# Kernel tuning notes

Measured on AMD Instinct MI355X. Metric: run time of the kernel, lower is better.

## Reference

```python
import jax, jax.numpy as jnp
import numpy as np

N = 1_000_000      # nodes
E = 8_000_000      # edges per relation
IN, HID, OUT = 25, 10, 5
GAT_SLOPE = 0.2    # GATv2Conv negative_slope default
ACT_SLOPE = 0.1    # module's LeakyReLU(0.1)


def setup_inputs() -> dict:
    key = jax.random.key(0)
    ks = jax.random.split(key, 40)
    d = {}
    d["x"] = jax.random.normal(ks[0], (N, IN), dtype=jnp.float32)
    for i, s in enumerate("psv"):
        d[f"edge_index_{s}"] = jax.random.randint(ks[1 + i], (2, E), 0, N, dtype=jnp.int32)
    # GATv2Conv params per relation: lin_l (source), lin_r (target), attention vec, bias
    k = 4
    for s in "psv":
        d[f"Wl_{s}"] = jax.random.normal(ks[k], (IN, OUT), jnp.float32) * 0.2; k += 1
        d[f"Wr_{s}"] = jax.random.normal(ks[k], (IN, OUT), jnp.float32) * 0.2; k += 1
        d[f"att_{s}"] = jax.random.normal(ks[k], (OUT,), jnp.float32) * 0.2; k += 1
        d[f"b_{s}"] = jnp.zeros((OUT,), jnp.float32)
    # projection: Linear(15,10) -> LeakyReLU(0.1) -> Linear(10,5)
    d["Wp1"] = jax.random.normal(ks[k], (3 * OUT, 2 * OUT), jnp.float32) * 0.2; k += 1
    d["bp1"] = jnp.zeros((2 * OUT,), jnp.float32)
    d["Wp2"] = jax.random.normal(ks[k], (2 * OUT, OUT), jnp.float32) * 0.2; k += 1
    d["bp2"] = jnp.zeros((OUT,), jnp.float32)
    # classifier: Linear(5,5) -> LeakyReLU(0.1) -> Linear(5,2)
    d["Wc1"] = jax.random.normal(ks[k], (OUT, OUT), jnp.float32) * 0.2; k += 1
    d["bc1"] = jnp.zeros((OUT,), jnp.float32)
    d["Wc2"] = jax.random.normal(ks[k], (OUT, 2), jnp.float32) * 0.2; k += 1
    d["bc2"] = jnp.zeros((2,), jnp.float32)
    return d


def lrelu(v, slope):
    return jnp.where(v >= 0, v, slope * v)


def gatv2_conv(x, edge_index, Wl, Wr, att, bias):
    """Single-head GATv2Conv with self-loops (PyG defaults)."""
    loops = jnp.arange(N, dtype=edge_index.dtype)
    src = jnp.concatenate([edge_index[0], loops])  # message sources j
    dst = jnp.concatenate([edge_index[1], loops])  # message targets i
    xl = x @ Wl  # [N, OUT] source transform (also message value)
    xr = x @ Wr  # [N, OUT] target transform
    # per-edge attention logits: a^T LeakyReLU(xl[j] + xr[i])
    e = lrelu(xl[src] + xr[dst], GAT_SLOPE) @ att  # [E+N]
    # segment softmax over incoming edges of each target node
    m = jax.ops.segment_max(e, dst, num_segments=N)
    ex = jnp.exp(e - m[dst])
    denom = jax.ops.segment_sum(ex, dst, num_segments=N)
    alpha = ex / denom[dst]
    out = jax.ops.segment_sum(alpha[:, None] * xl[src], dst, num_segments=N)
    return out + bias


def reference(x, edge_index_p, edge_index_s, edge_index_v,
              Wl_p, Wr_p, att_p, b_p,
              Wl_s, Wr_s, att_s, b_s,
              Wl_v, Wr_v, att_v, b_v,
              Wp1, bp1, Wp2, bp2, Wc1, bc1, Wc2, bc2):
    xp = lrelu(gatv2_conv(x, edge_index_p, Wl_p, Wr_p, att_p, b_p), ACT_SLOPE)
    xs = lrelu(gatv2_conv(x, edge_index_s, Wl_s, Wr_s, att_s, b_s), ACT_SLOPE)
    xv = lrelu(gatv2_conv(x, edge_index_v, Wl_v, Wr_v, att_v, b_v), ACT_SLOPE)
    h = jnp.concatenate([xp, xs, xv], axis=1)            # [N, 15]
    h = lrelu(h @ Wp1 + bp1, ACT_SLOPE) @ Wp2 + bp2      # projection (dropout=0)
    h = lrelu(h @ Wc1 + bc1, ACT_SLOPE) @ Wc2 + bc2      # classifier
    return h  # [N, 2]
```

## Files before the change

### kernel.cpp

```cpp
#include <hip/hip_runtime.h>

static constexpr int KIN  = 25;
static constexpr int KOUT = 5;
static constexpr int NBLK = 512;
static constexpr int BTH  = 1024;
static constexpr int BSH  = 9;
static constexpr int NPB  = 1 << BSH;
static constexpr int NBH  = 2048;
static constexpr int BROW = NBH + 1;
static constexpr int CAP  = 5120;

__global__ __launch_bounds__(256) void k_node1(
    const float* __restrict__ x,
    const float* __restrict__ Wl, const float* __restrict__ Wr,
    float* __restrict__ xl8, float* __restrict__ xr5, int n)
{
    __shared__ float sWl[KIN * KOUT];
    __shared__ float sWr[KIN * KOUT];
    __shared__ float sx[256 * KIN];

    const int tid = threadIdx.x;
    if (tid < KIN * KOUT) { sWl[tid] = Wl[tid]; sWr[tid] = Wr[tid]; }

    const int base = blockIdx.x * 256;
    const int cnt  = min(256, n - base);
    const size_t xbase = (size_t)base * KIN;
    for (int i = tid; i < cnt * KIN; i += 256) sx[i] = x[xbase + i];
    __syncthreads();

    if (tid >= cnt) return;
    const int node = base + tid;

    float xls[KOUT] = {0.f, 0.f, 0.f, 0.f, 0.f};
    float xrs[KOUT] = {0.f, 0.f, 0.f, 0.f, 0.f};
    const float* xp = &sx[tid * KIN];
#pragma unroll
    for (int i = 0; i < KIN; ++i) {
        const float xv = xp[i];
#pragma unroll
        for (int o = 0; o < KOUT; ++o) {
            xls[o] += xv * sWl[i * KOUT + o];
            xrs[o] += xv * sWr[i * KOUT + o];
        }
    }

    const size_t n8 = (size_t)node * 8;
    float4 v4;
    v4.x = xls[0]; v4.y = xls[1]; v4.z = xls[2]; v4.w = xls[3];
    *(float4*)(xl8 + n8) = v4;
    xl8[n8 + 4] = xls[4];
    const size_t n5 = (size_t)node * 5;
#pragma unroll
    for (int o = 0; o < KOUT; ++o) xr5[n5 + o] = xrs[o];
}

__global__ __launch_bounds__(256) void k_node3(
    const float* __restrict__ x,
    const float* __restrict__ Wl0, const float* __restrict__ Wr0,
    const float* __restrict__ Wl1, const float* __restrict__ Wr1,
    const float* __restrict__ Wl2, const float* __restrict__ Wr2,
    float* __restrict__ xl8, float* __restrict__ xr5,
    int n)
{
    __shared__ float sWl[3][KIN * KOUT];
    __shared__ float sWr[3][KIN * KOUT];
    __shared__ float sx[256 * KIN];

    const int tid = threadIdx.x;
    if (tid < KIN * KOUT) {
        sWl[0][tid] = Wl0[tid]; sWr[0][tid] = Wr0[tid];
        sWl[1][tid] = Wl1[tid]; sWr[1][tid] = Wr1[tid];
        sWl[2][tid] = Wl2[tid]; sWr[2][tid] = Wr2[tid];
    }

    const int base = blockIdx.x * 256;
    const int cnt  = min(256, n - base);
    const size_t xbase = (size_t)base * KIN;
    for (int i = tid; i < cnt * KIN; i += 256) sx[i] = x[xbase + i];
    __syncthreads();

    if (tid >= cnt) return;
    const int node = base + tid;

    float xls[3][KOUT] = {};
    float xrs[3][KOUT] = {};
    const float* xp = &sx[tid * KIN];
#pragma unroll
    for (int i = 0; i < KIN; ++i) {
        const float xv = xp[i];
#pragma unroll
        for (int r = 0; r < 3; ++r)
#pragma unroll
            for (int o = 0; o < KOUT; ++o) {
                xls[r][o] += xv * sWl[r][i * KOUT + o];
                xrs[r][o] += xv * sWr[r][i * KOUT + o];
            }
    }

#pragma unroll
    for (int r = 0; r < 3; ++r) {
        const size_t n8 = (size_t)r * n * 8 + (size_t)node * 8;
        float4 v4;
        v4.x = xls[r][0]; v4.y = xls[r][1]; v4.z = xls[r][2]; v4.w = xls[r][3];
        *(float4*)(xl8 + n8) = v4;
        xl8[n8 + 4] = xls[r][4];
        const size_t n5 = (size_t)r * n * 5 + (size_t)node * 5;
#pragma unroll
        for (int o = 0; o < KOUT; ++o) xr5[n5 + o] = xrs[r][o];
    }
}

__global__ __launch_bounds__(BTH) void k_hist3(
    const int* __restrict__ d0p, const int* __restrict__ d1p,
    const int* __restrict__ d2p, int E, int NB, int* __restrict__ hist3)
{
    __shared__ int h[NBH];
    const int rel = blockIdx.y, b = blockIdx.x, tid = threadIdx.x;
    const int* dst = (rel == 0) ? d0p : (rel == 1 ? d1p : d2p);
    int* hist_blk = hist3 + (size_t)rel * NBLK * NBH;

    for (int i = tid; i < NB; i += BTH) h[i] = 0;
    __syncthreads();
    const int chunk = (E + NBLK - 1) / NBLK;
    const int eb = b * chunk, ee = min(E, eb + chunk);
    for (int i = eb + tid; i < ee; i += BTH)
        atomicAdd(&h[dst[i] >> BSH], 1);
    __syncthreads();
    for (int i = tid; i < NB; i += BTH) hist_blk[b * NBH + i] = h[i];
}

__global__ __launch_bounds__(256) void k_sumoffs3(
    int* __restrict__ hist3, int NB, int* __restrict__ totals3)
{
    const int rel = blockIdx.y;
    int* hist_blk = hist3 + (size_t)rel * NBLK * NBH;
    int* totals   = totals3 + rel * NBH;
    const int i = blockIdx.x * 256 + threadIdx.x;
    if (i >= NB) return;
    int s = 0;
    for (int b = 0; b < NBLK; ++b) {
        const int t = hist_blk[b * NBH + i];
        hist_blk[b * NBH + i] = s;
        s += t;
    }
    totals[i] = s;
}

__global__ __launch_bounds__(1024) void k_scan3(
    const int* __restrict__ totals3, int E, int NB, int* __restrict__ base3)
{
    __shared__ int s[1024];
    const int rel = blockIdx.x;
    const int* totals = totals3 + rel * NBH;
    int* base = base3 + rel * BROW;

    const int t = threadIdx.x;
    const int i0 = 2 * t, i1 = 2 * t + 1;
    const int t0 = (i0 < NB) ? totals[i0] : 0;
    const int t1 = (i1 < NB) ? totals[i1] : 0;
    const int pair = t0 + t1;
    s[t] = pair;
    __syncthreads();
    for (int off = 1; off < 1024; off <<= 1) {
        int v = (t >= off) ? s[t - off] : 0;
        __syncthreads();
        s[t] += v;
        __syncthreads();
    }
    const int excl = s[t] - pair;
    base[i0] = excl;
    base[i1] = excl + t0;
    if (t == 1023) base[NBH] = E;
}

__global__ __launch_bounds__(BTH) void k_scatter3(
    const int* __restrict__ s0p, const int* __restrict__ s1p,
    const int* __restrict__ s2p,
    const int* __restrict__ d0p, const int* __restrict__ d1p,
    const int* __restrict__ d2p,
    int E, int NB,
    const int* __restrict__ hist3, const int* __restrict__ base3,
    int* __restrict__ rs3)
{
    __shared__ int cur[NBH];
    const int rel = blockIdx.y, b = blockIdx.x, tid = threadIdx.x;
    const int* src = (rel == 0) ? s0p : (rel == 1 ? s1p : s2p);
    const int* dst = (rel == 0) ? d0p : (rel == 1 ? d1p : d2p);
    const int* hist_blk = hist3 + (size_t)rel * NBLK * NBH;
    const int* base = base3 + rel * BROW;
    int* rs = rs3 + (size_t)rel * E;

    for (int i = tid; i < NB; i += BTH)
        cur[i] = base[i] + hist_blk[b * NBH + i];
    __syncthreads();
    const int chunk = (E + NBLK - 1) / NBLK;
    const int eb = b * chunk, ee = min(E, eb + chunk);
    for (int i = eb + tid; i < ee; i += BTH) {
        const int d = dst[i];
        const int bkt = d >> BSH;
        const int pos = atomicAdd(&cur[bkt], 1);
        rs[pos] = (src[i] << BSH) | (d & (NPB - 1));
    }
}

template <int NREL>
__global__ __launch_bounds__(256) void k_gather4(
    const int* __restrict__ rs3, const int* __restrict__ base3,
    const float* __restrict__ xl8a, const float* __restrict__ xr5a,
    const float* __restrict__ at0, const float* __restrict__ at1,
    const float* __restrict__ at2,
    const float* __restrict__ bi0, const float* __restrict__ bi1,
    const float* __restrict__ bi2,
    float* __restrict__ xouta, int n, int E)
{
    __shared__ float acc[NPB][6];
    __shared__ float xrw[NPB * 5];
    __shared__ int   cur[NPB];
    __shared__ int   sorted[CAP];
    __shared__ int   sc[256];

    const int bx  = blockIdx.x;
    const int rel = (NREL == 1) ? 0 : bx % NREL;
    const int bkt = (NREL == 1) ? bx : bx / NREL;

    const int*   rs   = rs3 + (size_t)rel * E;
    const int*   base = base3 + rel * BROW;
    const float* xl8  = xl8a + (size_t)rel * 8 * n;
    const float* xr5  = xr5a + (size_t)rel * 5 * n;
    const float* att  = (rel == 0) ? at0 : (rel == 1 ? at1 : at2);
    const float* bias = (rel == 0) ? bi0 : (rel == 1 ? bi1 : bi2);
    float*       xout = xouta + (size_t)rel * 5 * n;

    const int tid = threadIdx.x;
    const int node0 = bkt << BSH;
    const int nn = min(NPB, n - node0);

    for (int i = tid; i < NPB * 6; i += 256) ((float*)acc)[i] = 0.f;
    for (int i = tid; i < nn * 5; i += 256) xrw[i] = xr5[(size_t)node0 * 5 + i];
    for (int i = tid; i < NPB; i += 256) cur[i] = 0;
    __syncthreads();

    const float a0 = att[0], a1 = att[1], a2 = att[2], a3 = att[3], a4 = att[4];
    const int eb = base[bkt], ee = base[bkt + 1];
    const int seg = ee - eb;

    if (seg > 0 && seg <= CAP) {
        for (int i = eb + tid; i < ee; i += 256)
            atomicAdd(&cur[rs[i] & (NPB - 1)], 1);
        __syncthreads();
        const int h0 = cur[2 * tid], h1 = cur[2 * tid + 1];
        const int pair = h0 + h1;
        sc[tid] = pair;
        __syncthreads();
        for (int off = 1; off < 256; off <<= 1) {
            const int v = (tid >= off) ? sc[tid - off] : 0;
            __syncthreads();
            sc[tid] += v;
            __syncthreads();
        }
        const int excl = sc[tid] - pair;
        cur[2 * tid] = excl;
        cur[2 * tid + 1] = excl + h0;
        __syncthreads();
        for (int i = eb + tid; i < ee; i += 256) {
            const int v = rs[i];
            const int p = atomicAdd(&cur[v & (NPB - 1)], 1);
            sorted[p] = v;
        }
        __syncthreads();
        const int C  = (seg + 255) / 256;
        const int s0 = tid * C;
        const int s1 = min(seg, s0 + C);
        int curdl = -1;
        float A0 = 0.f, A1 = 0.f, A2 = 0.f, A3 = 0.f, A4 = 0.f, A5 = 0.f;
        float xr0 = 0.f, xr1 = 0.f, xr2 = 0.f, xr3 = 0.f, xr4 = 0.f;
        for (int i = s0; i < s1; ++i) {
            const int v  = sorted[i];
            const int dl = v & (NPB - 1);
            const int s  = v >> BSH;
            const size_t s8 = (size_t)s * 8;
            const float4 xs = *(const float4*)(xl8 + s8);
            const float  xs4 = xl8[s8 + 4];
            if (dl != curdl) {
                if (curdl >= 0) {
                    atomicAdd(&acc[curdl][0], A0);
                    atomicAdd(&acc[curdl][1], A1);
                    atomicAdd(&acc[curdl][2], A2);
                    atomicAdd(&acc[curdl][3], A3);
                    atomicAdd(&acc[curdl][4], A4);
                    atomicAdd(&acc[curdl][5], A5);
                }
                curdl = dl;
                A0 = A1 = A2 = A3 = A4 = A5 = 0.f;
                const float* xr = &xrw[dl * 5];
                xr0 = xr[0]; xr1 = xr[1]; xr2 = xr[2]; xr3 = xr[3]; xr4 = xr[4];
            }
            float t, lg = 0.f;
            t = xs.x + xr0; t = (t >= 0.f) ? t : 0.2f * t; lg += t * a0;
            t = xs.y + xr1; t = (t >= 0.f) ? t : 0.2f * t; lg += t * a1;
            t = xs.z + xr2; t = (t >= 0.f) ? t : 0.2f * t; lg += t * a2;
            t = xs.w + xr3; t = (t >= 0.f) ? t : 0.2f * t; lg += t * a3;
            t = xs4  + xr4; t = (t >= 0.f) ? t : 0.2f * t; lg += t * a4;
            const float w = __expf(lg);
            A0 += w * xs.x; A1 += w * xs.y; A2 += w * xs.z;
            A3 += w * xs.w; A4 += w * xs4;  A5 += w;
        }
        if (curdl >= 0) {
            atomicAdd(&acc[curdl][0], A0);
            atomicAdd(&acc[curdl][1], A1);
            atomicAdd(&acc[curdl][2], A2);
            atomicAdd(&acc[curdl][3], A3);
            atomicAdd(&acc[curdl][4], A4);
            atomicAdd(&acc[curdl][5], A5);
        }
        __syncthreads();
    } else if (seg > CAP) {
        for (int i = eb + tid; i < ee; i += 256) {
            const int v  = rs[i];
            const int s  = v >> BSH;
            const int dl = v & (NPB - 1);
            const size_t s8 = (size_t)s * 8;
            const float4 xs = *(const float4*)(xl8 + s8);
            const float  xs4 = xl8[s8 + 4];
            const float* xr = &xrw[dl * 5];
            float t, lg = 0.f;
            t = xs.x + xr[0]; t = (t >= 0.f) ? t : 0.2f * t; lg += t * a0;
            t = xs.y + xr[1]; t = (t >= 0.f) ? t : 0.2f * t; lg += t * a1;
            t = xs.z + xr[2]; t = (t >= 0.f) ? t : 0.2f * t; lg += t * a2;
            t = xs.w + xr[3]; t = (t >= 0.f) ? t : 0.2f * t; lg += t * a3;
            t = xs4  + xr[4]; t = (t >= 0.f) ? t : 0.2f * t; lg += t * a4;
            const float w = __expf(lg);
            atomicAdd(&acc[dl][0], w * xs.x);
            atomicAdd(&acc[dl][1], w * xs.y);
            atomicAdd(&acc[dl][2], w * xs.z);
            atomicAdd(&acc[dl][3], w * xs.w);
            atomicAdd(&acc[dl][4], w * xs4);
            atomicAdd(&acc[dl][5], w);
        }
        __syncthreads();
    } else {
        __syncthreads();
    }

    const float b0 = bias[0], b1 = bias[1], b2 = bias[2], b3 = bias[3], b4 = bias[4];
    for (int l = tid; l < nn; l += 256) {
        const int node = node0 + l;
        const size_t s8 = (size_t)node * 8;
        const float4 xs = *(const float4*)(xl8 + s8);
        const float  xs4 = xl8[s8 + 4];
        const float* xr = &xrw[l * 5];

        float t, lg = 0.f;
        t = xs.x + xr[0]; t = (t >= 0.f) ? t : 0.2f * t; lg += t * a0;
        t = xs.y + xr[1]; t = (t >= 0.f) ? t : 0.2f * t; lg += t * a1;
        t = xs.z + xr[2]; t = (t >= 0.f) ? t : 0.2f * t; lg += t * a2;
        t = xs.w + xr[3]; t = (t >= 0.f) ? t : 0.2f * t; lg += t * a3;
        t = xs4  + xr[4]; t = (t >= 0.f) ? t : 0.2f * t; lg += t * a4;
        const float w = __expf(lg);

        const size_t d5 = (size_t)node * 5;
        const float inv = 1.0f / (acc[l][5] + w);
        float v;
        v = (acc[l][0] + w * xs.x) * inv + b0; xout[d5 + 0] = (v >= 0.f) ? v : 0.1f * v;
        v = (acc[l][1] + w * xs.y) * inv + b1; xout[d5 + 1] = (v >= 0.f) ? v : 0.1f * v;
        v = (acc[l][2] + w * xs.z) * inv + b2; xout[d5 + 2] = (v >= 0.f) ? v : 0.1f * v;
        v = (acc[l][3] + w * xs.w) * inv + b3; xout[d5 + 3] = (v >= 0.f) ? v : 0.1f * v;
        v = (acc[l][4] + w * xs4 ) * inv + b4; xout[d5 + 4] = (v >= 0.f) ? v : 0.1f * v;
    }
}

__global__ __launch_bounds__(256) void k_mlp(
    const float* __restrict__ xp, const float* __restrict__ xs,
    const float* __restrict__ xv,
    const float* __restrict__ Wp1, const float* __restrict__ bp1,
    const float* __restrict__ Wp2, const float* __restrict__ bp2,
    const float* __restrict__ Wc1, const float* __restrict__ bc1,
    const float* __restrict__ Wc2, const float* __restrict__ bc2,
    float* __restrict__ out, int n)
{
    __shared__ float sW[257];
    const int tid = threadIdx.x;
    if (tid < 150) sW[tid] = Wp1[tid];
    if (tid < 10)  sW[150 + tid] = bp1[tid];
    if (tid < 50)  sW[160 + tid] = Wp2[tid];
    if (tid < 5)   sW[210 + tid] = bp2[tid];
    if (tid < 25)  sW[215 + tid] = Wc1[tid];
    if (tid < 5)   sW[240 + tid] = bc1[tid];
    if (tid < 10)  sW[245 + tid] = Wc2[tid];
    if (tid < 2)   sW[255 + tid] = bc2[tid];
    __syncthreads();

    const int node = blockIdx.x * 256 + tid;
    if (node >= n) return;
    const size_t n5 = (size_t)node * KOUT;

    float h[15];
#pragma unroll
    for (int k = 0; k < 5; ++k) {
        h[k]      = xp[n5 + k];
        h[5 + k]  = xs[n5 + k];
        h[10 + k] = xv[n5 + k];
    }

    float t1[10];
#pragma unroll
    for (int o = 0; o < 10; ++o) {
        float a = sW[150 + o];
#pragma unroll
        for (int i = 0; i < 15; ++i) a += h[i] * sW[i * 10 + o];
        t1[o] = (a >= 0.f) ? a : 0.1f * a;
    }

    float t2[5];
#pragma unroll
    for (int o = 0; o < 5; ++o) {
        float a = sW[210 + o];
#pragma unroll
        for (int i = 0; i < 10; ++i) a += t1[i] * sW[160 + i * 5 + o];
        t2[o] = a;
    }

    float t3[5];
#pragma unroll
    for (int o = 0; o < 5; ++o) {
        float a = sW[240 + o];
#pragma unroll
        for (int i = 0; i < 5; ++i) a += t2[i] * sW[215 + i * 5 + o];
        t3[o] = (a >= 0.f) ? a : 0.1f * a;
    }

    float o0 = sW[255], o1 = sW[256];
#pragma unroll
    for (int i = 0; i < 5; ++i) {
        o0 += t3[i] * sW[245 + i * 2 + 0];
        o1 += t3[i] * sW[245 + i * 2 + 1];
    }
    out[(size_t)node * 2 + 0] = o0;
    out[(size_t)node * 2 + 1] = o1;
}

extern "C" void kernel_launch(void* const* d_in, const int* in_sizes, int n_in,
                              void* d_out, int out_size, void* d_ws, size_t ws_size,
                              hipStream_t stream)
{
    const float* x = (const float*)d_in[0];
    const int n = in_sizes[0] / KIN;
    const int E = in_sizes[1] / 2;
    const int NB = (n + NPB - 1) >> BSH;

    const int* ei[3] = { (const int*)d_in[1], (const int*)d_in[2], (const int*)d_in[3] };
    const float *Wl[3], *Wr[3], *att[3], *bias[3];
    for (int r = 0; r < 3; ++r) {
        const int base = 4 + r * 4;
        Wl[r]   = (const float*)d_in[base + 0];
        Wr[r]   = (const float*)d_in[base + 1];
        att[r]  = (const float*)d_in[base + 2];
        bias[r] = (const float*)d_in[base + 3];
    }
    const float* Wp1 = (const float*)d_in[16];
    const float* bp1 = (const float*)d_in[17];
    const float* Wp2 = (const float*)d_in[18];
    const float* bp2 = (const float*)d_in[19];
    const float* Wc1 = (const float*)d_in[20];
    const float* bc1 = (const float*)d_in[21];
    const float* Wc2 = (const float*)d_in[22];
    const float* bc2 = (const float*)d_in[23];

    const size_t intsA = (size_t)3 * E + 3 * NBH + 3 * BROW;
    const size_t need_A = ((size_t)54 * n + intsA) * 4;
    const bool fused = ws_size >= need_A;

    float* ws   = (float*)d_ws;
    float* xout = ws;
    float* xl8  = ws + (size_t)15 * n;
    float* xr5  = xl8 + (fused ? (size_t)24 * n : (size_t)8 * n);
    int*   rs3  = (int*)(xr5 + (fused ? (size_t)15 * n : (size_t)5 * n));
    int*   totals3 = rs3 + (fused ? (size_t)3 * E : (size_t)E);
    int*   base3   = totals3 + (fused ? 3 * NBH : NBH);
    int*   hist3   = (int*)(xout + (size_t)10 * n);

    const int nb_node = (n + 255) / 256;
    const int nb_cols = (NB + 255) / 256;

    if (fused) {
        k_node3<<<nb_node, 256, 0, stream>>>(x, Wl[0], Wr[0], Wl[1], Wr[1],
                                             Wl[2], Wr[2], xl8, xr5, n);
        k_hist3   <<<dim3(NBLK, 3),    BTH,  0, stream>>>(ei[0] + E, ei[1] + E,
                                                          ei[2] + E, E, NB, hist3);
        k_sumoffs3<<<dim3(nb_cols, 3), 256,  0, stream>>>(hist3, NB, totals3);
        k_scan3   <<<3,                1024, 0, stream>>>(totals3, E, NB, base3);
        k_scatter3<<<dim3(NBLK, 3),    BTH,  0, stream>>>(
            ei[0], ei[1], ei[2], ei[0] + E, ei[1] + E, ei[2] + E,
            E, NB, hist3, base3, rs3);
        k_gather4<3><<<3 * NB, 256, 0, stream>>>(
            rs3, base3, xl8, xr5,
            att[0], att[1], att[2], bias[0], bias[1], bias[2],
            xout, n, E);
    } else {
        for (int r = 0; r < 3; ++r) {
            float* xo = xout + (size_t)r * 5 * n;
            k_node1<<<nb_node, 256, 0, stream>>>(x, Wl[r], Wr[r], xl8, xr5, n);
            k_hist3   <<<dim3(NBLK, 1),    BTH,  0, stream>>>(ei[r] + E, ei[r] + E,
                                                              ei[r] + E, E, NB, hist3);
            k_sumoffs3<<<dim3(nb_cols, 1), 256,  0, stream>>>(hist3, NB, totals3);
            k_scan3   <<<1,                1024, 0, stream>>>(totals3, E, NB, base3);
            k_scatter3<<<dim3(NBLK, 1),    BTH,  0, stream>>>(
                ei[r], ei[r], ei[r], ei[r] + E, ei[r] + E, ei[r] + E,
                E, NB, hist3, base3, rs3);
            k_gather4<1><<<NB, 256, 0, stream>>>(
                rs3, base3, xl8, xr5,
                att[r], att[r], att[r], bias[r], bias[r], bias[r],
                xo, n, E);
        }
    }

    k_mlp<<<nb_node, 256, 0, stream>>>(xout, xout + (size_t)5 * n, xout + (size_t)10 * n,
                                       Wp1, bp1, Wp2, bp2, Wc1, bc1, Wc2, bc2,
                                       (float*)d_out, n);
}
```

Measured before the change: 1.116 ms.

## Fuse node transform into histogram kernel and vectorize edge loads

Merges the node-projection kernel into the histogram kernel as extra blocks, so the compute-bound projection can overlap with the atomic-bound histogram and one launch is removed. Histogram and scatter now read dst/src as int4, with chunks rounded to multiples of four so the vector loads stay aligned. The gather block mapping changes from interleaved relations to relation-major order. Risks include the fused kernel's larger shared footprint and 1024-thread blocks for the node work lowering occupancy, and 4x-unrolled scatter atomics changing contention patterns.

```diff
diff --git a/kernel.cpp b/kernel.cpp
--- a/kernel.cpp
+++ b/kernel.cpp
@@ -54,79 +54,91 @@
     for (int o = 0; o < KOUT; ++o) xr5[n5 + o] = xrs[o];
 }
 
-__global__ __launch_bounds__(256) void k_node3(
+__global__ __launch_bounds__(BTH) void k_histnode(
+    const int* __restrict__ d0p, const int* __restrict__ d1p,
+    const int* __restrict__ d2p, int E, int NB, int* __restrict__ hist3,
     const float* __restrict__ x,
     const float* __restrict__ Wl0, const float* __restrict__ Wr0,
     const float* __restrict__ Wl1, const float* __restrict__ Wr1,
     const float* __restrict__ Wl2, const float* __restrict__ Wr2,
-    float* __restrict__ xl8, float* __restrict__ xr5,
-    int n)
-{
-    __shared__ float sWl[3][KIN * KOUT];
-    __shared__ float sWr[3][KIN * KOUT];
-    __shared__ float sx[256 * KIN];
-
-    const int tid = threadIdx.x;
+    float* __restrict__ xl8, float* __restrict__ xr5, int n, int NNB)
+{
+    __shared__ float smem[7424];
+    const int y = blockIdx.y, bx = blockIdx.x, tid = threadIdx.x;
+
+    if (bx < NBLK) {
+        int* h = (int*)smem;
+        const int* dst = (y == 0) ? d0p : (y == 1 ? d1p : d2p);
+        int* hist_blk = hist3 + (size_t)y * NBLK * NBH;
+        for (int i = tid; i < NB; i += BTH) h[i] = 0;
+        __syncthreads();
+        const int chunk = (((E + NBLK - 1) / NBLK) + 3) & ~3;
+        const int eb = bx * chunk, ee = min(E, eb + chunk);
+        const int vend = eb + ((ee - eb) & ~3);
+        for (int i = eb + tid * 4; i < vend; i += BTH * 4) {
+            const int4 d4 = *(const int4*)(dst + i);
+            atomicAdd(&h[d4.x >> BSH], 1);
+            atomicAdd(&h[d4.y >> BSH], 1);
+            atomicAdd(&h[d4.z >> BSH], 1);
+            atomicAdd(&h[d4.w >> BSH], 1);
+        }
+        for (int i = vend + tid; i < ee; i += BTH)
+            atomicAdd(&h[dst[i] >> BSH], 1);
+        __syncthreads();
+        for (int i = tid; i < NB; i += BTH) hist_blk[bx * NBH + i] = h[i];
+        return;
+    }
+
+    if (y != 0) return;
+    const int g = bx - NBLK;
+    if (g >= NNB) return;
+
+    float* sW = smem;
+    float* sx = smem + 768;
     if (tid < KIN * KOUT) {
-        sWl[0][tid] = Wl0[tid]; sWr[0][tid] = Wr0[tid];
-        sWl[1][tid] = Wl1[tid]; sWr[1][tid] = Wr1[tid];
-        sWl[2][tid] = Wl2[tid]; sWr[2][tid] = Wr2[tid];
-    }
-
-    const int base = blockIdx.x * 256;
-    const int cnt  = min(256, n - base);
-    const size_t xbase = (size_t)base * KIN;
-    for (int i = tid; i < cnt * KIN; i += 256) sx[i] = x[xbase + i];
-    __syncthreads();
-
-    if (tid >= cnt) return;
-    const int node = base + tid;
-
-    float xls[3][KOUT] = {};
-    float xrs[3][KOUT] = {};
-    const float* xp = &sx[tid * KIN];
-#pragma unroll
-    for (int i = 0; i < KIN; ++i) {
-        const float xv = xp[i];
-#pragma unroll
-        for (int r = 0; r < 3; ++r)
-#pragma unroll
-            for (int o = 0; o < KOUT; ++o) {
-                xls[r][o] += xv * sWl[r][i * KOUT + o];
-                xrs[r][o] += xv * sWr[r][i * KOUT + o];
+        sW[tid]       = Wl0[tid]; sW[125 + tid] = Wr0[tid];
+        sW[250 + tid] = Wl1[tid]; sW[375 + tid] = Wr1[tid];
+        sW[500 + tid] = Wl2[tid]; sW[625 + tid] = Wr2[tid];
+    }
+
+    for (int sub = 0; sub < 4; ++sub) {
+        const int base = g * 1024 + sub * 256;
+        if (base >= n) break;
+        const int cnt = min(256, n - base);
+        __syncthreads();
+        const size_t xb = (size_t)base * KIN;
+        for (int i = tid; i < cnt * KIN; i += BTH) sx[i] = x[xb + i];
+        __syncthreads();
+        if (tid < cnt) {
+            const int node = base + tid;
+            float xls[3][KOUT] = {};
+            float xrs[3][KOUT] = {};
+            const float* xp = &sx[tid * KIN];
+#pragma unroll
+            for (int i = 0; i < KIN; ++i) {
+                const float xv = xp[i];
+#pragma unroll
+                for (int r = 0; r < 3; ++r)
+#pragma unroll
+                    for (int o = 0; o < KOUT; ++o) {
+                        xls[r][o] += xv * sW[r * 250 + i * KOUT + o];
+                        xrs[r][o] += xv * sW[r * 250 + 125 + i * KOUT + o];
+                    }
             }
-    }
-
-#pragma unroll
-    for (int r = 0; r < 3; ++r) {
-        const size_t n8 = (size_t)r * n * 8 + (size_t)node * 8;
-        float4 v4;
-        v4.x = xls[r][0]; v4.y = xls[r][1]; v4.z = xls[r][2]; v4.w = xls[r][3];
-        *(float4*)(xl8 + n8) = v4;
-        xl8[n8 + 4] = xls[r][4];
-        const size_t n5 = (size_t)r * n * 5 + (size_t)node * 5;
-#pragma unroll
-        for (int o = 0; o < KOUT; ++o) xr5[n5 + o] = xrs[r][o];
-    }
-}
-
-__global__ __launch_bounds__(BTH) void k_hist3(
-    const int* __restrict__ d0p, const int* __restrict__ d1p,
-    const int* __restrict__ d2p, int E, int NB, int* __restrict__ hist3)
-{
-    __shared__ int h[NBH];
-    const int rel = blockIdx.y, b = blockIdx.x, tid = threadIdx.x;
-    const int* dst = (rel == 0) ? d0p : (rel == 1 ? d1p : d2p);
-    int* hist_blk = hist3 + (size_t)rel * NBLK * NBH;
-
-    for (int i = tid; i < NB; i += BTH) h[i] = 0;
-    __syncthreads();
-    const int chunk = (E + NBLK - 1) / NBLK;
-    const int eb = b * chunk, ee = min(E, eb + chunk);
-    for (int i = eb + tid; i < ee; i += BTH)
-        atomicAdd(&h[dst[i] >> BSH], 1);
-    __syncthreads();
-    for (int i = tid; i < NB; i += BTH) hist_blk[b * NBH + i] = h[i];
+#pragma unroll
+            for (int r = 0; r < 3; ++r) {
+                const size_t n8 = (size_t)r * n * 8 + (size_t)node * 8;
+                float4 v4;
+                v4.x = xls[r][0]; v4.y = xls[r][1];
+                v4.z = xls[r][2]; v4.w = xls[r][3];
+                *(float4*)(xl8 + n8) = v4;
+                xl8[n8 + 4] = xls[r][4];
+                const size_t n5 = (size_t)r * n * 5 + (size_t)node * 5;
+#pragma unroll
+                for (int o = 0; o < KOUT; ++o) xr5[n5 + o] = xrs[r][o];
+            }
+        }
+    }
 }
 
 __global__ __launch_bounds__(256) void k_sumoffs3(
@@ -193,12 +205,21 @@
     for (int i = tid; i < NB; i += BTH)
         cur[i] = base[i] + hist_blk[b * NBH + i];
     __syncthreads();
-    const int chunk = (E + NBLK - 1) / NBLK;
+    const int chunk = (((E + NBLK - 1) / NBLK) + 3) & ~3;
     const int eb = b * chunk, ee = min(E, eb + chunk);
-    for (int i = eb + tid; i < ee; i += BTH) {
+    const int vend = eb + ((ee - eb) & ~3);
+    for (int i = eb + tid * 4; i < vend; i += BTH * 4) {
+        const int4 s4 = *(const int4*)(src + i);
+        const int4 d4 = *(const int4*)(dst + i);
+        int p;
+        p = atomicAdd(&cur[d4.x >> BSH], 1); rs[p] = (s4.x << BSH) | (d4.x & (NPB - 1));
+        p = atomicAdd(&cur[d4.y >> BSH], 1); rs[p] = (s4.y << BSH) | (d4.y & (NPB - 1));
+        p = atomicAdd(&cur[d4.z >> BSH], 1); rs[p] = (s4.z << BSH) | (d4.z & (NPB - 1));
+        p = atomicAdd(&cur[d4.w >> BSH], 1); rs[p] = (s4.w << BSH) | (d4.w & (NPB - 1));
+    }
+    for (int i = vend + tid; i < ee; i += BTH) {
         const int d = dst[i];
-        const int bkt = d >> BSH;
-        const int pos = atomicAdd(&cur[bkt], 1);
+        const int pos = atomicAdd(&cur[d >> BSH], 1);
         rs[pos] = (src[i] << BSH) | (d & (NPB - 1));
     }
 }
@@ -211,7 +232,7 @@
     const float* __restrict__ at2,
     const float* __restrict__ bi0, const float* __restrict__ bi1,
     const float* __restrict__ bi2,
-    float* __restrict__ xouta, int n, int E)
+    float* __restrict__ xouta, int n, int E, int NB)
 {
     __shared__ float acc[NPB][6];
     __shared__ float xrw[NPB * 5];
@@ -220,8 +241,8 @@
     __shared__ int   sc[256];
 
     const int bx  = blockIdx.x;
-    const int rel = (NREL == 1) ? 0 : bx % NREL;
-    const int bkt = (NREL == 1) ? bx : bx / NREL;
+    const int rel = (NREL == 1) ? 0 : bx / NB;
+    const int bkt = (NREL == 1) ? bx : bx % NB;
 
     const int*   rs   = rs3 + (size_t)rel * E;
     const int*   base = base3 + rel * BROW;
@@ -481,12 +502,12 @@
 
     const int nb_node = (n + 255) / 256;
     const int nb_cols = (NB + 255) / 256;
+    const int NNB     = (n + 1023) / 1024;
 
     if (fused) {
-        k_node3<<<nb_node, 256, 0, stream>>>(x, Wl[0], Wr[0], Wl[1], Wr[1],
-                                             Wl[2], Wr[2], xl8, xr5, n);
-        k_hist3   <<<dim3(NBLK, 3),    BTH,  0, stream>>>(ei[0] + E, ei[1] + E,
-                                                          ei[2] + E, E, NB, hist3);
+        k_histnode<<<dim3(NBLK + NNB, 3), BTH, 0, stream>>>(
+            ei[0] + E, ei[1] + E, ei[2] + E, E, NB, hist3,
+            x, Wl[0], Wr[0], Wl[1], Wr[1], Wl[2], Wr[2], xl8, xr5, n, NNB);
         k_sumoffs3<<<dim3(nb_cols, 3), 256,  0, stream>>>(hist3, NB, totals3);
         k_scan3   <<<3,                1024, 0, stream>>>(totals3, E, NB, base3);
         k_scatter3<<<dim3(NBLK, 3),    BTH,  0, stream>>>(
@@ -495,13 +516,14 @@
         k_gather4<3><<<3 * NB, 256, 0, stream>>>(
             rs3, base3, xl8, xr5,
             att[0], att[1], att[2], bias[0], bias[1], bias[2],
-            xout, n, E);
+            xout, n, E, NB);
     } else {
         for (int r = 0; r < 3; ++r) {
             float* xo = xout + (size_t)r * 5 * n;
             k_node1<<<nb_node, 256, 0, stream>>>(x, Wl[r], Wr[r], xl8, xr5, n);
-            k_hist3   <<<dim3(NBLK, 1),    BTH,  0, stream>>>(ei[r] + E, ei[r] + E,
-                                                              ei[r] + E, E, NB, hist3);
+            k_histnode<<<dim3(NBLK, 1), BTH, 0, stream>>>(
+                ei[r] + E, ei[r] + E, ei[r] + E, E, NB, hist3,
+                x, Wl[r], Wr[r], Wl[r], Wr[r], Wl[r], Wr[r], xl8, xr5, n, 0);
             k_sumoffs3<<<dim3(nb_cols, 1), 256,  0, stream>>>(hist3, NB, totals3);
             k_scan3   <<<1,                1024, 0, stream>>>(totals3, E, NB, base3);
             k_scatter3<<<dim3(NBLK, 1),    BTH,  0, stream>>>(
@@ -510,7 +532,7 @@
             k_gather4<1><<<NB, 256, 0, stream>>>(
                 rs3, base3, xl8, xr5,
                 att[r], att[r], att[r], bias[r], bias[r], bias[r],
-                xo, n, E);
+                xo, n, E, NB);
         }
     }
 
```

New measurement: 1.066 ms. -4.6%, faster.
